# Optimization experiments

Hardware: AMD Instinct MI355X
Metric: run time of the kernel (lower is better)

Reference implementation:

```python
import jax, jax.numpy as jnp
import numpy as np

N = 50000          # nodes
E = 800000         # edges (avg degree 16)
H, D = 4, 32       # heads, per-head channels; hidden = H*D = 128
DIMS_IN = [32, 128, 128]


def setup_inputs() -> dict:
    key = jax.random.key(0)
    ks = jax.random.split(key, 40)
    inp = {}
    inp["x"] = jax.random.normal(ks[0], (N, 32), jnp.float32)
    inp["edge_index"] = jax.random.randint(ks[1], (2, E), 0, N, dtype=jnp.int32)
    i = 2
    for l, din in enumerate(DIMS_IN):
        for nm in ["q", "k", "v", "s"]:
            inp[f"W{nm}{l}"] = jax.random.normal(ks[i], (din, H * D), jnp.float32) / np.float32(np.sqrt(din)); i += 1
            inp[f"b{nm}{l}"] = jax.random.normal(ks[i], (H * D,), jnp.float32) * 0.01; i += 1
    inp["Wf"] = jax.random.normal(ks[i], (H * D, 1), jnp.float32) / np.float32(np.sqrt(H * D)); i += 1
    inp["bf"] = jax.random.normal(ks[i], (1,), jnp.float32) * 0.01
    return inp


def _transformer_conv(x, src, dst, Wq, bq, Wk, bk, Wv, bv, Ws, bs):
    """PyG TransformerConv (concat=True, root_weight=True, beta=False, eval mode)."""
    n = x.shape[0]
    q = (x @ Wq + bq).reshape(n, H, D)   # queries at nodes
    k = (x @ Wk + bk).reshape(n, H, D)
    v = (x @ Wv + bv).reshape(n, H, D)
    # per-edge attention score: q at destination, k at source
    s = jnp.einsum("ehd,ehd->eh", q[dst], k[src]) / np.float32(np.sqrt(D))  # [E,H]
    # segment softmax over incoming edges of each destination node
    m = jax.ops.segment_max(s, dst, num_segments=n)          # [N,H]
    e = jnp.exp(s - m[dst])                                  # [E,H]
    den = jax.ops.segment_sum(e, dst, num_segments=n)        # [N,H]
    alpha = e / den[dst]                                     # [E,H]
    agg = jax.ops.segment_sum(alpha[:, :, None] * v[src], dst, num_segments=n)  # [N,H,D]
    return agg.reshape(n, H * D) + (x @ Ws + bs)             # skip connection


def reference(x, edge_index,
              Wq0, bq0, Wk0, bk0, Wv0, bv0, Ws0, bs0,
              Wq1, bq1, Wk1, bk1, Wv1, bv1, Ws1, bs1,
              Wq2, bq2, Wk2, bk2, Wv2, bv2, Ws2, bs2,
              Wf, bf):
    src, dst = edge_index[0], edge_index[1]
    layers = [
        (Wq0, bq0, Wk0, bk0, Wv0, bv0, Ws0, bs0),
        (Wq1, bq1, Wk1, bk1, Wv1, bv1, Ws1, bs1),
        (Wq2, bq2, Wk2, bk2, Wv2, bv2, Ws2, bs2),
    ]
    h = x
    for p in layers:
        h = jax.nn.relu(_transformer_conv(h, src, dst, *p))
    out = jax.nn.sigmoid(h @ Wf + bf)  # [N,1]
    return out
```

## Files before the change

kernel.cpp:

```cpp
#include <hip/hip_runtime.h>
#include <hip/hip_bf16.h>
#include <cstdint>
#include <cstddef>

typedef __attribute__((ext_vector_type(8))) short bf16x8;
typedef __attribute__((ext_vector_type(4))) float f32x4;
typedef __attribute__((ext_vector_type(2))) float f32x2;

#define MAXD 64

__device__ __forceinline__ unsigned short f2bs(float f){
  __hip_bfloat16 h = __float2bfloat16(f);
  return *(unsigned short*)&h;
}
__device__ __forceinline__ unsigned short f2bs_trunc(float f){
  return (unsigned short)(__float_as_uint(f) >> 16);
}
__device__ __forceinline__ float bflo(unsigned int u){ return __uint_as_float(u << 16); }
__device__ __forceinline__ float bfhi(unsigned int u){ return __uint_as_float(u & 0xffff0000u); }
__device__ __forceinline__ f32x2 b2f2(unsigned int u){
  return (f32x2){ __uint_as_float(u << 16), __uint_as_float(u & 0xffff0000u) };
}

struct PrepArgs {
  const float* w[8];
  unsigned short* o[8];
  int* cnt;
  int n;
};

__global__ void prep_kernel(PrepArgs a){
  int m = blockIdx.y;
  if (m < 8){
    int e = blockIdx.x*256 + threadIdx.x;
    int n  = e >> 6;
    int k2 = e & 63;
    const float* W = a.w[m];
    unsigned int lo = __float_as_uint(W[(2*k2)  *128 + n]) >> 16;
    unsigned int hi = __float_as_uint(W[(2*k2+1)*128 + n]) & 0xffff0000u;
    ((unsigned int*)a.o[m])[e] = lo | hi;
  } else {
    for (int i = blockIdx.x*256 + threadIdx.x; i < a.n; i += 32*256) a.cnt[i] = 0;
  }
}

__global__ __launch_bounds__(256)
void scatter_gemm0(const int* __restrict__ src, const int* __restrict__ dst, int E,
                   int* __restrict__ cnt, int* __restrict__ adj, int SB, int gb,
                   const float* __restrict__ x, int nn,
                   const float* __restrict__ W0, const float* __restrict__ W1,
                   const float* __restrict__ W2, const float* __restrict__ W3,
                   const float* __restrict__ b0, const float* __restrict__ b1,
                   const float* __restrict__ b2, const float* __restrict__ b3,
                   unsigned short* __restrict__ Q, unsigned short* __restrict__ KV,
                   unsigned short* __restrict__ S)
{
  __shared__ __align__(16) unsigned short wt[128*40];
  int t = threadIdx.x;
  if ((int)blockIdx.x < SB){
    int e = blockIdx.x*256 + t;
    if (e < E){
      int d = dst[e];
      int slot = atomicAdd(&cnt[d], 1);
      if (slot < MAXD) adj[d*MAXD + slot] = src[e];
    }
    return;
  }
  int b2i  = blockIdx.x - SB;
  int msel = b2i / gb;
  int tile = b2i % gb;
  const float* W = (msel==0)?W0:(msel==1)?W1:(msel==2)?W2:W3;
  const float* B = (msel==0)?b0:(msel==1)?b1:(msel==2)?b2:b3;

  for (int idx = t; idx < 4096; idx += 256){
    int k = idx >> 7, n = idx & 127;
    wt[n*40 + k] = f2bs_trunc(W[k*128 + n]);
  }

  int lane = t & 63, wv = t >> 6;
  int m0 = tile*64 + wv*16;
  int n16 = lane & 15, quad = lane >> 4;

  int arow = min(m0 + n16, nn-1);
  const float* xr = x + (size_t)arow*32 + quad*8;
  float4 a0 = *(const float4*)xr;
  float4 a1 = *(const float4*)(xr + 4);
  bf16x8 af;
  af[0]=(short)f2bs_trunc(a0.x); af[1]=(short)f2bs_trunc(a0.y);
  af[2]=(short)f2bs_trunc(a0.z); af[3]=(short)f2bs_trunc(a0.w);
  af[4]=(short)f2bs_trunc(a1.x); af[5]=(short)f2bs_trunc(a1.y);
  af[6]=(short)f2bs_trunc(a1.z); af[7]=(short)f2bs_trunc(a1.w);

  __syncthreads();

  f32x4 acc[8];
  #pragma unroll
  for (int c=0;c<8;c++) acc[c] = (f32x4){0.f,0.f,0.f,0.f};
  #pragma unroll
  for (int c = 0; c < 8; c++){
    bf16x8 bf = *(const bf16x8*)&wt[(c*16 + n16)*40 + quad*8];
    acc[c] = __builtin_amdgcn_mfma_f32_16x16x32_bf16(af, bf, acc[c], 0, 0, 0);
  }

  unsigned short* O = (msel==0) ? Q : (msel==3) ? S : KV;
  int ostride = (msel==1 || msel==2) ? 256 : 128;
  int ooff    = (msel==2) ? 128 : 0;
  #pragma unroll
  for (int c = 0; c < 8; c++){
    int col = c*16 + n16;
    float bias = B[col];
    #pragma unroll
    for (int r = 0; r < 4; r++){
      int row = m0 + quad*4 + r;
      if (row < nn) O[(size_t)row*ostride + ooff + col] = f2bs(acc[c][r] + bias);
    }
  }
}

__global__ __launch_bounds__(256)
void gemm4_mfma(const unsigned short* __restrict__ X, int nn,
                const unsigned short* __restrict__ T0, const unsigned short* __restrict__ T1,
                const unsigned short* __restrict__ T2, const unsigned short* __restrict__ T3,
                const float* __restrict__ b0, const float* __restrict__ b1,
                const float* __restrict__ b2, const float* __restrict__ b3,
                unsigned short* __restrict__ Q, unsigned short* __restrict__ KV,
                unsigned short* __restrict__ S)
{
  constexpr int DIN = 128, KP = DIN + 8;
  __shared__ __align__(16) unsigned short wt[128*KP];
  int t = threadIdx.x;
  int msel = blockIdx.y;
  const unsigned short* WT = (msel==0)?T0:(msel==1)?T1:(msel==2)?T2:T3;
  const float* B = (msel==0)?b0:(msel==1)?b1:(msel==2)?b2:b3;

  {
    const int NU = 128*DIN/8;
    for (int u = t; u < NU; u += 256){
      uint4 v = ((const uint4*)WT)[u];
      int n = u / (DIN/8), b = u % (DIN/8);
      *(uint4*)&wt[n*KP + b*8] = v;
    }
  }

  int lane = t & 63, wv = t >> 6;
  int m0 = blockIdx.x*64 + wv*16;
  int n16 = lane & 15, quad = lane >> 4;

  bf16x8 af[DIN/32];
  {
    const unsigned short* xrow = X + (size_t)(m0 + n16)*DIN + quad*8;
    #pragma unroll
    for (int s = 0; s < DIN/32; s++) af[s] = *(const bf16x8*)(xrow + s*32);
  }

  __syncthreads();

  f32x4 acc[8];
  #pragma unroll
  for (int c=0;c<8;c++) acc[c] = (f32x4){0.f,0.f,0.f,0.f};
  #pragma unroll
  for (int s = 0; s < DIN/32; s++){
    #pragma unroll
    for (int c = 0; c < 8; c++){
      bf16x8 bf = *(const bf16x8*)&wt[(c*16 + n16)*KP + s*32 + quad*8];
      acc[c] = __builtin_amdgcn_mfma_f32_16x16x32_bf16(af[s], bf, acc[c], 0, 0, 0);
    }
  }

  unsigned short* O = (msel==0) ? Q : (msel==3) ? S : KV;
  int ostride = (msel==1 || msel==2) ? 256 : 128;
  int ooff    = (msel==2) ? 128 : 0;
  #pragma unroll
  for (int c = 0; c < 8; c++){
    int col = c*16 + n16;
    float bias = B[col];
    #pragma unroll
    for (int r = 0; r < 4; r++){
      int row = m0 + quad*4 + r;
      if (row < nn) O[(size_t)row*ostride + ooff + col] = f2bs(acc[c][r] + bias);
    }
  }
}

template<bool FINAL>
__global__ __launch_bounds__(256)
void attn_kernel(const unsigned short* __restrict__ q,  const unsigned short* __restrict__ kv,
                 const unsigned short* __restrict__ skip,
                 const int* __restrict__ cnt, const int* __restrict__ adj,
                 unsigned short* __restrict__ hout,
                 const float* __restrict__ Wf, const float* __restrict__ bfp,
                 float* __restrict__ out, int nn)
{
  int lane = threadIdx.x & 63, wid = threadIdx.x >> 6;
  int n = blockIdx.x*4 + wid;
  if (n >= nn) return;
  int p = lane & 15, g = lane >> 4;
  const float RS = 0.17677669529663687f;

  f32x2 qv[4];
  { uint4 qu = *(const uint4*)(q + (size_t)n*128 + p*8);
    qv[0]=b2f2(qu.x); qv[1]=b2f2(qu.y); qv[2]=b2f2(qu.z); qv[3]=b2f2(qu.w); }

  int dg = min(cnt[n], MAXD);
  float m = -INFINITY, l = 0.f;
  f32x2 acc[4] = {{0.f,0.f},{0.f,0.f},{0.f,0.f},{0.f,0.f}};

  if (dg > 0){
    int cn = dg;
    int idx = adj[n*MAXD + min(lane, cn-1)];
    int nit = (cn + 7) >> 3;

    bool a0 = 2*g < cn, a1 = 2*g + 1 < cn;
    int s0 = __shfl(idx, min(2*g    , cn-1), 64);
    int s1 = __shfl(idx, min(2*g + 1, cn-1), 64);
    uint4 ku0 = *(const uint4*)(kv + (size_t)s0*256 + p*8);
    uint4 ku1 = *(const uint4*)(kv + (size_t)s1*256 + p*8);
    uint4 vu0 = *(const uint4*)(kv + (size_t)s0*256 + 128 + p*8);
    uint4 vu1 = *(const uint4*)(kv + (size_t)s1*256 + 128 + p*8);

    for (int it = 0; it < nit; ++it){
      int jn0 = (it+1)*8 + 2*g;
      bool b0 = jn0 < cn, b1 = jn0 + 1 < cn;
      int t0 = __shfl(idx, min(jn0    , cn-1), 64);
      int t1 = __shfl(idx, min(jn0 + 1, cn-1), 64);
      uint4 kn0={0,0,0,0}, kn1={0,0,0,0}, vn0={0,0,0,0}, vn1={0,0,0,0};
      if (it + 1 < nit){
        kn0 = *(const uint4*)(kv + (size_t)t0*256 + p*8);
        kn1 = *(const uint4*)(kv + (size_t)t1*256 + p*8);
        vn0 = *(const uint4*)(kv + (size_t)t0*256 + 128 + p*8);
        vn1 = *(const uint4*)(kv + (size_t)t1*256 + 128 + p*8);
      }
      f32x2 d0v = qv[0]*b2f2(ku0.x);
      d0v = __builtin_elementwise_fma(qv[1], b2f2(ku0.y), d0v);
      d0v = __builtin_elementwise_fma(qv[2], b2f2(ku0.z), d0v);
      d0v = __builtin_elementwise_fma(qv[3], b2f2(ku0.w), d0v);
      f32x2 d1v = qv[0]*b2f2(ku1.x);
      d1v = __builtin_elementwise_fma(qv[1], b2f2(ku1.y), d1v);
      d1v = __builtin_elementwise_fma(qv[2], b2f2(ku1.z), d1v);
      d1v = __builtin_elementwise_fma(qv[3], b2f2(ku1.w), d1v);
      float d0 = d0v.x + d0v.y;
      float d1 = d1v.x + d1v.y;
      d0 += __shfl_xor(d0, 1, 64); d0 += __shfl_xor(d0, 2, 64);
      d1 += __shfl_xor(d1, 1, 64); d1 += __shfl_xor(d1, 2, 64);
      float f0 = a0 ? d0*RS : -INFINITY;
      float f1 = a1 ? d1*RS : -INFINITY;

      float nm = fmaxf(m, fmaxf(f0, f1));
      float r  = __expf(fmaxf(m  - nm, -80.f));
      float w0 = __expf(fmaxf(f0 - nm, -80.f));
      float w1 = __expf(fmaxf(f1 - nm, -80.f));
      m = nm;
      l = l*r + (w0 + w1);
      f32x2 rr  = {r , r };
      f32x2 w0v = {w0, w0};
      f32x2 w1v = {w1, w1};
      acc[0] = __builtin_elementwise_fma(w1v, b2f2(vu1.x),
               __builtin_elementwise_fma(w0v, b2f2(vu0.x), acc[0]*rr));
      acc[1] = __builtin_elementwise_fma(w1v, b2f2(vu1.y),
               __builtin_elementwise_fma(w0v, b2f2(vu0.y), acc[1]*rr));
      acc[2] = __builtin_elementwise_fma(w1v, b2f2(vu1.z),
               __builtin_elementwise_fma(w0v, b2f2(vu0.z), acc[2]*rr));
      acc[3] = __builtin_elementwise_fma(w1v, b2f2(vu1.w),
               __builtin_elementwise_fma(w0v, b2f2(vu0.w), acc[3]*rr));
      ku0=kn0; ku1=kn1; vu0=vn0; vu1=vn1; a0=b0; a1=b1;
    }
  }

  float m1 = fmaxf(m, __shfl_xor(m, 16, 64));
  float M  = fmaxf(m1, __shfl_xor(m1, 32, 64));
  float sc = __expf(fmaxf(m - M, -80.f));
  float lp = l * sc;
  lp += __shfl_xor(lp, 16, 64);
  float L = lp + __shfl_xor(lp, 32, 64);
  f32x2 scv = {sc, sc};
  float o[8];
  #pragma unroll
  for (int i=0;i<4;i++){
    f32x2 a = acc[i]*scv;
    a.x += __shfl_xor(a.x, 16, 64); a.y += __shfl_xor(a.y, 16, 64);
    a.x += __shfl_xor(a.x, 32, 64); a.y += __shfl_xor(a.y, 32, 64);
    o[2*i] = a.x; o[2*i+1] = a.y;
  }
  float inv = (L > 0.f) ? 1.f/L : 0.f;
  float sk[8];
  { uint4 su = *(const uint4*)(skip + (size_t)n*128 + p*8);
    sk[0]=bflo(su.x); sk[1]=bfhi(su.x); sk[2]=bflo(su.y); sk[3]=bfhi(su.y);
    sk[4]=bflo(su.z); sk[5]=bfhi(su.z); sk[6]=bflo(su.w); sk[7]=bfhi(su.w); }
  #pragma unroll
  for (int i=0;i<8;i++) o[i] = fmaxf(fmaf(o[i], inv, sk[i]), 0.f);

  if constexpr (!FINAL){
    if (g == 0){
      uint4 st;
      st.x = (unsigned)f2bs(o[0]) | ((unsigned)f2bs(o[1])<<16);
      st.y = (unsigned)f2bs(o[2]) | ((unsigned)f2bs(o[3])<<16);
      st.z = (unsigned)f2bs(o[4]) | ((unsigned)f2bs(o[5])<<16);
      st.w = (unsigned)f2bs(o[6]) | ((unsigned)f2bs(o[7])<<16);
      *(uint4*)(hout + (size_t)n*128 + p*8) = st;
    }
  } else {
    float4 w0 = *(const float4*)(Wf + p*8);
    float4 w1 = *(const float4*)(Wf + p*8 + 4);
    float pd = o[0]*w0.x;
    pd = fmaf(o[1], w0.y, pd); pd = fmaf(o[2], w0.z, pd); pd = fmaf(o[3], w0.w, pd);
    pd = fmaf(o[4], w1.x, pd); pd = fmaf(o[5], w1.y, pd);
    pd = fmaf(o[6], w1.z, pd); pd = fmaf(o[7], w1.w, pd);
    pd += __shfl_xor(pd, 1, 64);
    pd += __shfl_xor(pd, 2, 64);
    pd += __shfl_xor(pd, 4, 64);
    pd += __shfl_xor(pd, 8, 64);
    if (lane == 0){
      float z = pd + bfp[0];
      out[n] = 1.f / (1.f + __expf(-z));
    }
  }
}

extern "C" void kernel_launch(void* const* d_in, const int* in_sizes, int n_in,
                              void* d_out, int out_size, void* d_ws, size_t ws_size,
                              hipStream_t stream) {
  const int N = in_sizes[0] / 32;
  const int E = in_sizes[1] / 2;
  const float* x = (const float*)d_in[0];
  const int* ei  = (const int*)d_in[1];
  const int* src = ei;
  const int* dst = ei + E;
  auto Wp = [&](int i){ return (const float*)d_in[i]; };
  const int NP = N + 64;

  char* p = (char*)d_ws;
  auto alloc = [&](size_t b){ char* r = p; p += (b + 255) & ~(size_t)255; return (void*)r; };
  unsigned short* F0  = (unsigned short*)alloc((size_t)NP*128*2);
  unsigned short* F1  = (unsigned short*)alloc((size_t)NP*128*2);
  unsigned short* Qb  = (unsigned short*)alloc((size_t)NP*128*2);
  unsigned short* KVb = (unsigned short*)alloc((size_t)NP*256*2);
  unsigned short* WT[8];
  for (int i = 0; i < 8; i++) WT[i] = (unsigned short*)alloc((size_t)128*128*2);
  int* cnt = (int*)alloc((size_t)N*4);
  int* adj = (int*)alloc((size_t)N*MAXD*4);

  PrepArgs pa;
  const int widx[8] = {10,12,14,16, 18,20,22,24};
  for (int i = 0; i < 8; i++){ pa.w[i] = Wp(widx[i]); pa.o[i] = WT[i]; }
  pa.cnt = cnt; pa.n = N;
  prep_kernel<<<dim3(32,9), 256, 0, stream>>>(pa);

  int SB = (E + 255) / 256;
  int gb = (N + 63) / 64;
  int ab = (N + 3) / 4;

  scatter_gemm0<<<SB + 4*gb, 256, 0, stream>>>(src, dst, E, cnt, adj, SB, gb,
      x, N, Wp(2),Wp(4),Wp(6),Wp(8), Wp(3),Wp(5),Wp(7),Wp(9), Qb, KVb, F0);
  attn_kernel<false><<<ab, 256, 0, stream>>>(Qb, KVb, F0, cnt, adj, F0,
      nullptr, nullptr, nullptr, N);
  gemm4_mfma<<<dim3(gb,4), 256, 0, stream>>>(F0, N,
      WT[0],WT[1],WT[2],WT[3], Wp(11),Wp(13),Wp(15),Wp(17), Qb, KVb, F1);
  attn_kernel<false><<<ab, 256, 0, stream>>>(Qb, KVb, F1, cnt, adj, F1,
      nullptr, nullptr, nullptr, N);
  gemm4_mfma<<<dim3(gb,4), 256, 0, stream>>>(F1, N,
      WT[4],WT[5],WT[6],WT[7], Wp(19),Wp(21),Wp(23),Wp(25), Qb, KVb, F0);
  attn_kernel<true><<<ab, 256, 0, stream>>>(Qb, KVb, F0, cnt, adj, nullptr,
      Wp(26), Wp(27), (float*)d_out, N);
}
```

Before: 416.3 us.

## Fuse all layers into one persistent cooperative kernel with grid syncs

Replaces the seven separate launches (weight prep, scatter plus first GEMM, three attention passes, two GEMMs) with a single cooperative kernel. Blocks grid-stride through each phase and are separated by grid.sync barriers. The aim is to remove per-launch overhead and the tail idle between kernels. In exchange, the grid is capped by occupancy, at most 4 blocks per CU with a 34 KB LDS buffer held throughout. That may reduce latency hiding in the gather-heavy attention phases, and each grid-wide barrier adds its own cost.

```diff
diff --git a/kernel.cpp b/kernel.cpp
--- a/kernel.cpp
+++ b/kernel.cpp
@@ -1,7 +1,10 @@
 #include <hip/hip_runtime.h>
+#include <hip/hip_cooperative_groups.h>
 #include <hip/hip_bf16.h>
 #include <cstdint>
 #include <cstddef>
+
+namespace cg = cooperative_groups;
 
 typedef __attribute__((ext_vector_type(8))) short bf16x8;
 typedef __attribute__((ext_vector_type(4))) float f32x4;
@@ -22,61 +25,29 @@
   return (f32x2){ __uint_as_float(u << 16), __uint_as_float(u & 0xffff0000u) };
 }
 
-struct PrepArgs {
-  const float* w[8];
-  unsigned short* o[8];
-  int* cnt;
-  int n;
+struct MegaArgs {
+  const int* src; const int* dst; int E;
+  const float* x; int N;
+  const float* W0[4]; const float* B0[4];
+  const float* W12[8];
+  const float* B1[4]; const float* B2[4];
+  unsigned short* WT[8];
+  const float* Wf; const float* bfp;
+  unsigned short *F0, *F1, *Q, *KV;
+  int* cnt; int* adj;
+  float* out;
 };
 
-__global__ void prep_kernel(PrepArgs a){
-  int m = blockIdx.y;
-  if (m < 8){
-    int e = blockIdx.x*256 + threadIdx.x;
-    int n  = e >> 6;
-    int k2 = e & 63;
-    const float* W = a.w[m];
-    unsigned int lo = __float_as_uint(W[(2*k2)  *128 + n]) >> 16;
-    unsigned int hi = __float_as_uint(W[(2*k2+1)*128 + n]) & 0xffff0000u;
-    ((unsigned int*)a.o[m])[e] = lo | hi;
-  } else {
-    for (int i = blockIdx.x*256 + threadIdx.x; i < a.n; i += 32*256) a.cnt[i] = 0;
-  }
-}
-
-__global__ __launch_bounds__(256)
-void scatter_gemm0(const int* __restrict__ src, const int* __restrict__ dst, int E,
-                   int* __restrict__ cnt, int* __restrict__ adj, int SB, int gb,
-                   const float* __restrict__ x, int nn,
-                   const float* __restrict__ W0, const float* __restrict__ W1,
-                   const float* __restrict__ W2, const float* __restrict__ W3,
-                   const float* __restrict__ b0, const float* __restrict__ b1,
-                   const float* __restrict__ b2, const float* __restrict__ b3,
-                   unsigned short* __restrict__ Q, unsigned short* __restrict__ KV,
-                   unsigned short* __restrict__ S)
+__device__ __forceinline__ void gemm0_tile(unsigned short* wt, const float* __restrict__ x, int nn,
+    const float* __restrict__ W, const float* __restrict__ B,
+    unsigned short* __restrict__ O, int ostride, int ooff, int tile)
 {
-  __shared__ __align__(16) unsigned short wt[128*40];
   int t = threadIdx.x;
-  if ((int)blockIdx.x < SB){
-    int e = blockIdx.x*256 + t;
-    if (e < E){
-      int d = dst[e];
-      int slot = atomicAdd(&cnt[d], 1);
-      if (slot < MAXD) adj[d*MAXD + slot] = src[e];
-    }
-    return;
-  }
-  int b2i  = blockIdx.x - SB;
-  int msel = b2i / gb;
-  int tile = b2i % gb;
-  const float* W = (msel==0)?W0:(msel==1)?W1:(msel==2)?W2:W3;
-  const float* B = (msel==0)?b0:(msel==1)?b1:(msel==2)?b2:b3;
-
+  __syncthreads();
   for (int idx = t; idx < 4096; idx += 256){
     int k = idx >> 7, n = idx & 127;
     wt[n*40 + k] = f2bs_trunc(W[k*128 + n]);
   }
-
   int lane = t & 63, wv = t >> 6;
   int m0 = tile*64 + wv*16;
   int n16 = lane & 15, quad = lane >> 4;
@@ -101,10 +72,6 @@
     bf16x8 bf = *(const bf16x8*)&wt[(c*16 + n16)*40 + quad*8];
     acc[c] = __builtin_amdgcn_mfma_f32_16x16x32_bf16(af, bf, acc[c], 0, 0, 0);
   }
-
-  unsigned short* O = (msel==0) ? Q : (msel==3) ? S : KV;
-  int ostride = (msel==1 || msel==2) ? 256 : 128;
-  int ooff    = (msel==2) ? 128 : 0;
   #pragma unroll
   for (int c = 0; c < 8; c++){
     int col = c*16 + n16;
@@ -117,59 +84,42 @@
   }
 }
 
-__global__ __launch_bounds__(256)
-void gemm4_mfma(const unsigned short* __restrict__ X, int nn,
-                const unsigned short* __restrict__ T0, const unsigned short* __restrict__ T1,
-                const unsigned short* __restrict__ T2, const unsigned short* __restrict__ T3,
-                const float* __restrict__ b0, const float* __restrict__ b1,
-                const float* __restrict__ b2, const float* __restrict__ b3,
-                unsigned short* __restrict__ Q, unsigned short* __restrict__ KV,
-                unsigned short* __restrict__ S)
+__device__ __forceinline__ void gemm128_tile(unsigned short* wt, const unsigned short* __restrict__ X,
+    int nn, const unsigned short* __restrict__ WT, const float* __restrict__ B,
+    unsigned short* __restrict__ O, int ostride, int ooff, int tile)
 {
-  constexpr int DIN = 128, KP = DIN + 8;
-  __shared__ __align__(16) unsigned short wt[128*KP];
   int t = threadIdx.x;
-  int msel = blockIdx.y;
-  const unsigned short* WT = (msel==0)?T0:(msel==1)?T1:(msel==2)?T2:T3;
-  const float* B = (msel==0)?b0:(msel==1)?b1:(msel==2)?b2:b3;
-
+  __syncthreads();
   {
-    const int NU = 128*DIN/8;
-    for (int u = t; u < NU; u += 256){
+    for (int u = t; u < 2048; u += 256){
       uint4 v = ((const uint4*)WT)[u];
-      int n = u / (DIN/8), b = u % (DIN/8);
-      *(uint4*)&wt[n*KP + b*8] = v;
-    }
-  }
-
+      int n = u >> 4, b = u & 15;
+      *(uint4*)&wt[n*136 + b*8] = v;
+    }
+  }
   int lane = t & 63, wv = t >> 6;
-  int m0 = blockIdx.x*64 + wv*16;
+  int m0 = tile*64 + wv*16;
   int n16 = lane & 15, quad = lane >> 4;
 
-  bf16x8 af[DIN/32];
+  bf16x8 af[4];
   {
-    const unsigned short* xrow = X + (size_t)(m0 + n16)*DIN + quad*8;
+    const unsigned short* xrow = X + (size_t)(m0 + n16)*128 + quad*8;
     #pragma unroll
-    for (int s = 0; s < DIN/32; s++) af[s] = *(const bf16x8*)(xrow + s*32);
-  }
-
+    for (int s = 0; s < 4; s++) af[s] = *(const bf16x8*)(xrow + s*32);
+  }
   __syncthreads();
 
   f32x4 acc[8];
   #pragma unroll
   for (int c=0;c<8;c++) acc[c] = (f32x4){0.f,0.f,0.f,0.f};
   #pragma unroll
-  for (int s = 0; s < DIN/32; s++){
+  for (int s = 0; s < 4; s++){
     #pragma unroll
     for (int c = 0; c < 8; c++){
-      bf16x8 bf = *(const bf16x8*)&wt[(c*16 + n16)*KP + s*32 + quad*8];
+      bf16x8 bf = *(const bf16x8*)&wt[(c*16 + n16)*136 + s*32 + quad*8];
       acc[c] = __builtin_amdgcn_mfma_f32_16x16x32_bf16(af[s], bf, acc[c], 0, 0, 0);
     }
   }
-
-  unsigned short* O = (msel==0) ? Q : (msel==3) ? S : KV;
-  int ostride = (msel==1 || msel==2) ? 256 : 128;
-  int ooff    = (msel==2) ? 128 : 0;
   #pragma unroll
   for (int c = 0; c < 8; c++){
     int col = c*16 + n16;
@@ -182,17 +132,13 @@
   }
 }
 
-template<bool FINAL>
-__global__ __launch_bounds__(256)
-void attn_kernel(const unsigned short* __restrict__ q,  const unsigned short* __restrict__ kv,
-                 const unsigned short* __restrict__ skip,
-                 const int* __restrict__ cnt, const int* __restrict__ adj,
-                 unsigned short* __restrict__ hout,
-                 const float* __restrict__ Wf, const float* __restrict__ bfp,
-                 float* __restrict__ out, int nn)
+__device__ __forceinline__ void attn_node(int n, int nn,
+    const unsigned short* __restrict__ q, const unsigned short* __restrict__ kv,
+    const unsigned short* __restrict__ skip, const int* __restrict__ cnt,
+    const int* __restrict__ adj, unsigned short* __restrict__ hout,
+    const float* __restrict__ Wf, const float* __restrict__ bfp,
+    float* __restrict__ out, bool final_, int lane)
 {
-  int lane = threadIdx.x & 63, wid = threadIdx.x >> 6;
-  int n = blockIdx.x*4 + wid;
   if (n >= nn) return;
   int p = lane & 15, g = lane >> 4;
   const float RS = 0.17677669529663687f;
@@ -276,10 +222,10 @@
   float o[8];
   #pragma unroll
   for (int i=0;i<4;i++){
-    f32x2 a = acc[i]*scv;
-    a.x += __shfl_xor(a.x, 16, 64); a.y += __shfl_xor(a.y, 16, 64);
-    a.x += __shfl_xor(a.x, 32, 64); a.y += __shfl_xor(a.y, 32, 64);
-    o[2*i] = a.x; o[2*i+1] = a.y;
+    f32x2 aa = acc[i]*scv;
+    aa.x += __shfl_xor(aa.x, 16, 64); aa.y += __shfl_xor(aa.y, 16, 64);
+    aa.x += __shfl_xor(aa.x, 32, 64); aa.y += __shfl_xor(aa.y, 32, 64);
+    o[2*i] = aa.x; o[2*i+1] = aa.y;
   }
   float inv = (L > 0.f) ? 1.f/L : 0.f;
   float sk[8];
@@ -289,7 +235,7 @@
   #pragma unroll
   for (int i=0;i<8;i++) o[i] = fmaxf(fmaf(o[i], inv, sk[i]), 0.f);
 
-  if constexpr (!FINAL){
+  if (!final_){
     if (g == 0){
       uint4 st;
       st.x = (unsigned)f2bs(o[0]) | ((unsigned)f2bs(o[1])<<16);
@@ -316,6 +262,81 @@
   }
 }
 
+__global__ __launch_bounds__(256, 4)
+void mega_kernel(MegaArgs a)
+{
+  __shared__ __align__(16) unsigned short wt[128*136];
+  cg::grid_group grid = cg::this_grid();
+  const int G = gridDim.x;
+  int t = threadIdx.x;
+  int lane = t & 63, wid = t >> 6;
+
+  for (int u = blockIdx.x*256 + t; u < 8*8192; u += G*256){
+    int m = u >> 13, e = u & 8191;
+    int n = e >> 6, k2 = e & 63;
+    const float* W = a.W12[m];
+    unsigned int lo = __float_as_uint(W[(2*k2)  *128 + n]) >> 16;
+    unsigned int hi = __float_as_uint(W[(2*k2+1)*128 + n]) & 0xffff0000u;
+    ((unsigned int*)a.WT[m])[e] = lo | hi;
+  }
+  for (int i = blockIdx.x*256 + t; i < a.N; i += G*256) a.cnt[i] = 0;
+  grid.sync();
+
+  int SB = (a.E + 255) >> 8;
+  int gb = (a.N + 63) >> 6;
+  for (int b = blockIdx.x; b < SB + 4*gb; b += G){
+    if (b < SB){
+      int e = b*256 + t;
+      if (e < a.E){
+        int d = a.dst[e];
+        int slot = atomicAdd(&a.cnt[d], 1);
+        if (slot < MAXD) a.adj[d*MAXD + slot] = a.src[e];
+      }
+    } else {
+      int b2 = b - SB;
+      int msel = b2 / gb, tile = b2 % gb;
+      unsigned short* O = (msel==0) ? a.Q : (msel==3) ? a.F0 : a.KV;
+      int ostride = (msel==1 || msel==2) ? 256 : 128;
+      int ooff    = (msel==2) ? 128 : 0;
+      gemm0_tile(wt, a.x, a.N, a.W0[msel], a.B0[msel], O, ostride, ooff, tile);
+    }
+  }
+  grid.sync();
+
+  int ab = (a.N + 3) >> 2;
+  for (int i = blockIdx.x; i < ab; i += G)
+    attn_node(i*4 + wid, a.N, a.Q, a.KV, a.F0, a.cnt, a.adj, a.F0,
+              nullptr, nullptr, nullptr, false, lane);
+  grid.sync();
+
+  for (int b = blockIdx.x; b < 4*gb; b += G){
+    int msel = b / gb, tile = b % gb;
+    unsigned short* O = (msel==0) ? a.Q : (msel==3) ? a.F1 : a.KV;
+    int ostride = (msel==1 || msel==2) ? 256 : 128;
+    int ooff    = (msel==2) ? 128 : 0;
+    gemm128_tile(wt, a.F0, a.N, a.WT[msel], a.B1[msel], O, ostride, ooff, tile);
+  }
+  grid.sync();
+
+  for (int i = blockIdx.x; i < ab; i += G)
+    attn_node(i*4 + wid, a.N, a.Q, a.KV, a.F1, a.cnt, a.adj, a.F1,
+              nullptr, nullptr, nullptr, false, lane);
+  grid.sync();
+
+  for (int b = blockIdx.x; b < 4*gb; b += G){
+    int msel = b / gb, tile = b % gb;
+    unsigned short* O = (msel==0) ? a.Q : (msel==3) ? a.F0 : a.KV;
+    int ostride = (msel==1 || msel==2) ? 256 : 128;
+    int ooff    = (msel==2) ? 128 : 0;
+    gemm128_tile(wt, a.F1, a.N, a.WT[4+msel], a.B2[msel], O, ostride, ooff, tile);
+  }
+  grid.sync();
+
+  for (int i = blockIdx.x; i < ab; i += G)
+    attn_node(i*4 + wid, a.N, a.Q, a.KV, a.F0, a.cnt, a.adj, nullptr,
+              a.Wf, a.bfp, a.out, true, lane);
+}
+
 extern "C" void kernel_launch(void* const* d_in, const int* in_sizes, int n_in,
                               void* d_out, int out_size, void* d_ws, size_t ws_size,
                               hipStream_t stream) {
@@ -323,8 +344,6 @@
   const int E = in_sizes[1] / 2;
   const float* x = (const float*)d_in[0];
   const int* ei  = (const int*)d_in[1];
-  const int* src = ei;
-  const int* dst = ei + E;
   auto Wp = [&](int i){ return (const float*)d_in[i]; };
   const int NP = N + 64;
 
@@ -339,26 +358,28 @@
   int* cnt = (int*)alloc((size_t)N*4);
   int* adj = (int*)alloc((size_t)N*MAXD*4);
 
-  PrepArgs pa;
-  const int widx[8] = {10,12,14,16, 18,20,22,24};
-  for (int i = 0; i < 8; i++){ pa.w[i] = Wp(widx[i]); pa.o[i] = WT[i]; }
-  pa.cnt = cnt; pa.n = N;
-  prep_kernel<<<dim3(32,9), 256, 0, stream>>>(pa);
-
-  int SB = (E + 255) / 256;
-  int gb = (N + 63) / 64;
-  int ab = (N + 3) / 4;
-
-  scatter_gemm0<<<SB + 4*gb, 256, 0, stream>>>(src, dst, E, cnt, adj, SB, gb,
-      x, N, Wp(2),Wp(4),Wp(6),Wp(8), Wp(3),Wp(5),Wp(7),Wp(9), Qb, KVb, F0);
-  attn_kernel<false><<<ab, 256, 0, stream>>>(Qb, KVb, F0, cnt, adj, F0,
-      nullptr, nullptr, nullptr, N);
-  gemm4_mfma<<<dim3(gb,4), 256, 0, stream>>>(F0, N,
-      WT[0],WT[1],WT[2],WT[3], Wp(11),Wp(13),Wp(15),Wp(17), Qb, KVb, F1);
-  attn_kernel<false><<<ab, 256, 0, stream>>>(Qb, KVb, F1, cnt, adj, F1,
-      nullptr, nullptr, nullptr, N);
-  gemm4_mfma<<<dim3(gb,4), 256, 0, stream>>>(F1, N,
-      WT[4],WT[5],WT[6],WT[7], Wp(19),Wp(21),Wp(23),Wp(25), Qb, KVb, F0);
-  attn_kernel<true><<<ab, 256, 0, stream>>>(Qb, KVb, F0, cnt, adj, nullptr,
-      Wp(26), Wp(27), (float*)d_out, N);
-}
+  MegaArgs ma;
+  ma.src = ei; ma.dst = ei + E; ma.E = E;
+  ma.x = x; ma.N = N;
+  const int w0i[4] = {2,4,6,8};
+  const int w1i[4] = {10,12,14,16};
+  const int w2i[4] = {18,20,22,24};
+  for (int i = 0; i < 4; i++){
+    ma.W0[i]  = Wp(w0i[i]); ma.B0[i] = Wp(w0i[i]+1);
+    ma.W12[i]   = Wp(w1i[i]); ma.B1[i] = Wp(w1i[i]+1);
+    ma.W12[4+i] = Wp(w2i[i]); ma.B2[i] = Wp(w2i[i]+1);
+  }
+  for (int i = 0; i < 8; i++) ma.WT[i] = WT[i];
+  ma.Wf = Wp(26); ma.bfp = Wp(27);
+  ma.F0 = F0; ma.F1 = F1; ma.Q = Qb; ma.KV = KVb;
+  ma.cnt = cnt; ma.adj = adj;
+  ma.out = (float*)d_out;
+
+  int maxB = 0;
+  hipOccupancyMaxActiveBlocksPerMultiprocessor(&maxB, mega_kernel, 256, 0);
+  int G = (maxB > 0) ? maxB * 256 : 768;
+  if (G > 2048) G = 2048;
+
+  void* params[] = { &ma };
+  hipLaunchCooperativeKernel((void*)mega_kernel, dim3(G), dim3(256), params, 0, stream);
+}
```

Result: slower. 898.6 us (+115.9%).

## Partition adjacency scatter by destination range and fold weight prep into fused kernel

Applied to the files above, without the earlier changes.

The edge scatter now has each block handle a 2048-edge chunk restricted to one of 8 destination-node ranges. Blocks working on the same range run close together, so atomics and adjacency writes are meant to stay in a narrower, more cache-friendly address window. The weight transpose/bf16 conversion for layers 1-2 moves into the same fused launch as the scatter and the layer-0 GEMM, and the counter zeroing becomes its own small kernel. The cost is that every edge's dst is read 8 times, which adds load traffic.

```diff
diff --git a/kernel.cpp b/kernel.cpp
--- a/kernel.cpp
+++ b/kernel.cpp
@@ -22,97 +22,110 @@
   return (f32x2){ __uint_as_float(u << 16), __uint_as_float(u & 0xffff0000u) };
 }
 
-struct PrepArgs {
-  const float* w[8];
-  unsigned short* o[8];
-  int* cnt;
-  int n;
+__global__ void zero_cnt_kernel(int* __restrict__ p, int n){
+  int i = blockIdx.x*256 + threadIdx.x;
+  if (i < n) p[i] = 0;
+}
+
+struct FatArgs {
+  const int* src; const int* dst; int E;
+  int* cnt; int* adj;
+  int SBP, GB;
+  const float* x; int N;
+  const float* W0[4]; const float* B0[4];
+  const float* W12[8];
+  unsigned short* WT[8];
+  unsigned short *Q, *KV, *S;
 };
 
-__global__ void prep_kernel(PrepArgs a){
-  int m = blockIdx.y;
-  if (m < 8){
-    int e = blockIdx.x*256 + threadIdx.x;
-    int n  = e >> 6;
-    int k2 = e & 63;
-    const float* W = a.w[m];
-    unsigned int lo = __float_as_uint(W[(2*k2)  *128 + n]) >> 16;
-    unsigned int hi = __float_as_uint(W[(2*k2+1)*128 + n]) & 0xffff0000u;
-    ((unsigned int*)a.o[m])[e] = lo | hi;
-  } else {
-    for (int i = blockIdx.x*256 + threadIdx.x; i < a.n; i += 32*256) a.cnt[i] = 0;
-  }
-}
-
 __global__ __launch_bounds__(256)
-void scatter_gemm0(const int* __restrict__ src, const int* __restrict__ dst, int E,
-                   int* __restrict__ cnt, int* __restrict__ adj, int SB, int gb,
-                   const float* __restrict__ x, int nn,
-                   const float* __restrict__ W0, const float* __restrict__ W1,
-                   const float* __restrict__ W2, const float* __restrict__ W3,
-                   const float* __restrict__ b0, const float* __restrict__ b1,
-                   const float* __restrict__ b2, const float* __restrict__ b3,
-                   unsigned short* __restrict__ Q, unsigned short* __restrict__ KV,
-                   unsigned short* __restrict__ S)
+void fat_kernel(FatArgs a)
 {
   __shared__ __align__(16) unsigned short wt[128*40];
   int t = threadIdx.x;
-  if ((int)blockIdx.x < SB){
-    int e = blockIdx.x*256 + t;
-    if (e < E){
-      int d = dst[e];
-      int slot = atomicAdd(&cnt[d], 1);
-      if (slot < MAXD) adj[d*MAXD + slot] = src[e];
+  int b = blockIdx.x;
+
+  if (b < a.SBP){
+    int p = b & 7, c = b >> 3;
+    int base = c*2048;
+    int plo = ( p      * a.N) / 8;
+    int phi = ((p + 1) * a.N) / 8;
+    #pragma unroll
+    for (int i = 0; i < 8; i++){
+      int e = base + t + i*256;
+      if (e < a.E){
+        int d = a.dst[e];
+        if (d >= plo && d < phi){
+          int slot = atomicAdd(&a.cnt[d], 1);
+          if (slot < MAXD) a.adj[d*MAXD + slot] = a.src[e];
+        }
+      }
     }
     return;
   }
-  int b2i  = blockIdx.x - SB;
-  int msel = b2i / gb;
-  int tile = b2i % gb;
-  const float* W = (msel==0)?W0:(msel==1)?W1:(msel==2)?W2:W3;
-  const float* B = (msel==0)?b0:(msel==1)?b1:(msel==2)?b2:b3;
-
-  for (int idx = t; idx < 4096; idx += 256){
-    int k = idx >> 7, n = idx & 127;
-    wt[n*40 + k] = f2bs_trunc(W[k*128 + n]);
-  }
-
-  int lane = t & 63, wv = t >> 6;
-  int m0 = tile*64 + wv*16;
-  int n16 = lane & 15, quad = lane >> 4;
-
-  int arow = min(m0 + n16, nn-1);
-  const float* xr = x + (size_t)arow*32 + quad*8;
-  float4 a0 = *(const float4*)xr;
-  float4 a1 = *(const float4*)(xr + 4);
-  bf16x8 af;
-  af[0]=(short)f2bs_trunc(a0.x); af[1]=(short)f2bs_trunc(a0.y);
-  af[2]=(short)f2bs_trunc(a0.z); af[3]=(short)f2bs_trunc(a0.w);
-  af[4]=(short)f2bs_trunc(a1.x); af[5]=(short)f2bs_trunc(a1.y);
-  af[6]=(short)f2bs_trunc(a1.z); af[7]=(short)f2bs_trunc(a1.w);
-
-  __syncthreads();
-
-  f32x4 acc[8];
-  #pragma unroll
-  for (int c=0;c<8;c++) acc[c] = (f32x4){0.f,0.f,0.f,0.f};
-  #pragma unroll
-  for (int c = 0; c < 8; c++){
-    bf16x8 bf = *(const bf16x8*)&wt[(c*16 + n16)*40 + quad*8];
-    acc[c] = __builtin_amdgcn_mfma_f32_16x16x32_bf16(af, bf, acc[c], 0, 0, 0);
-  }
-
-  unsigned short* O = (msel==0) ? Q : (msel==3) ? S : KV;
-  int ostride = (msel==1 || msel==2) ? 256 : 128;
-  int ooff    = (msel==2) ? 128 : 0;
-  #pragma unroll
-  for (int c = 0; c < 8; c++){
-    int col = c*16 + n16;
-    float bias = B[col];
-    #pragma unroll
-    for (int r = 0; r < 4; r++){
-      int row = m0 + quad*4 + r;
-      if (row < nn) O[(size_t)row*ostride + ooff + col] = f2bs(acc[c][r] + bias);
+  b -= a.SBP;
+
+  if (b < 4*a.GB){
+    int msel = b / a.GB, tile = b % a.GB;
+    const float* W = a.W0[msel];
+    const float* B = a.B0[msel];
+    for (int idx = t; idx < 4096; idx += 256){
+      int k = idx >> 7, n = idx & 127;
+      wt[n*40 + k] = f2bs_trunc(W[k*128 + n]);
+    }
+    int lane = t & 63, wv = t >> 6;
+    int m0 = tile*64 + wv*16;
+    int n16 = lane & 15, quad = lane >> 4;
+
+    int arow = min(m0 + n16, a.N-1);
+    const float* xr = a.x + (size_t)arow*32 + quad*8;
+    float4 a0 = *(const float4*)xr;
+    float4 a1 = *(const float4*)(xr + 4);
+    bf16x8 af;
+    af[0]=(short)f2bs_trunc(a0.x); af[1]=(short)f2bs_trunc(a0.y);
+    af[2]=(short)f2bs_trunc(a0.z); af[3]=(short)f2bs_trunc(a0.w);
+    af[4]=(short)f2bs_trunc(a1.x); af[5]=(short)f2bs_trunc(a1.y);
+    af[6]=(short)f2bs_trunc(a1.z); af[7]=(short)f2bs_trunc(a1.w);
+
+    __syncthreads();
+
+    f32x4 acc[8];
+    #pragma unroll
+    for (int c2=0;c2<8;c2++) acc[c2] = (f32x4){0.f,0.f,0.f,0.f};
+    #pragma unroll
+    for (int c2 = 0; c2 < 8; c2++){
+      bf16x8 bf = *(const bf16x8*)&wt[(c2*16 + n16)*40 + quad*8];
+      acc[c2] = __builtin_amdgcn_mfma_f32_16x16x32_bf16(af, bf, acc[c2], 0, 0, 0);
+    }
+
+    unsigned short* O = (msel==0) ? a.Q : (msel==3) ? a.S : a.KV;
+    int ostride = (msel==1 || msel==2) ? 256 : 128;
+    int ooff    = (msel==2) ? 128 : 0;
+    #pragma unroll
+    for (int c2 = 0; c2 < 8; c2++){
+      int col = c2*16 + n16;
+      float bias = B[col];
+      #pragma unroll
+      for (int r = 0; r < 4; r++){
+        int row = m0 + quad*4 + r;
+        if (row < a.N) O[(size_t)row*ostride + ooff + col] = f2bs(acc[c2][r] + bias);
+      }
+    }
+    return;
+  }
+  b -= 4*a.GB;
+
+  {
+    int m = b >> 2, part = b & 3;
+    const float* W = a.W12[m];
+    unsigned int* O = (unsigned int*)a.WT[m];
+    #pragma unroll
+    for (int i = 0; i < 8; i++){
+      int e = part*2048 + t + i*256;
+      int n = e >> 6, k2 = e & 63;
+      unsigned int lo = __float_as_uint(W[(2*k2)  *128 + n]) >> 16;
+      unsigned int hi = __float_as_uint(W[(2*k2+1)*128 + n]) & 0xffff0000u;
+      O[e] = lo | hi;
     }
   }
 }
@@ -276,10 +289,10 @@
   float o[8];
   #pragma unroll
   for (int i=0;i<4;i++){
-    f32x2 a = acc[i]*scv;
-    a.x += __shfl_xor(a.x, 16, 64); a.y += __shfl_xor(a.y, 16, 64);
-    a.x += __shfl_xor(a.x, 32, 64); a.y += __shfl_xor(a.y, 32, 64);
-    o[2*i] = a.x; o[2*i+1] = a.y;
+    f32x2 aa = acc[i]*scv;
+    aa.x += __shfl_xor(aa.x, 16, 64); aa.y += __shfl_xor(aa.y, 16, 64);
+    aa.x += __shfl_xor(aa.x, 32, 64); aa.y += __shfl_xor(aa.y, 32, 64);
+    o[2*i] = aa.x; o[2*i+1] = aa.y;
   }
   float inv = (L > 0.f) ? 1.f/L : 0.f;
   float sk[8];
@@ -323,8 +336,6 @@
   const int E = in_sizes[1] / 2;
   const float* x = (const float*)d_in[0];
   const int* ei  = (const int*)d_in[1];
-  const int* src = ei;
-  const int* dst = ei + E;
   auto Wp = [&](int i){ return (const float*)d_in[i]; };
   const int NP = N + 64;
 
@@ -339,18 +350,29 @@
   int* cnt = (int*)alloc((size_t)N*4);
   int* adj = (int*)alloc((size_t)N*MAXD*4);
 
-  PrepArgs pa;
-  const int widx[8] = {10,12,14,16, 18,20,22,24};
-  for (int i = 0; i < 8; i++){ pa.w[i] = Wp(widx[i]); pa.o[i] = WT[i]; }
-  pa.cnt = cnt; pa.n = N;
-  prep_kernel<<<dim3(32,9), 256, 0, stream>>>(pa);
-
-  int SB = (E + 255) / 256;
-  int gb = (N + 63) / 64;
+  zero_cnt_kernel<<<(N+255)/256, 256, 0, stream>>>(cnt, N);
+
+  FatArgs fa;
+  fa.src = ei; fa.dst = ei + E; fa.E = E;
+  fa.cnt = cnt; fa.adj = adj;
+  int chunks = (E + 2047) / 2048;
+  fa.SBP = chunks * 8;
+  fa.GB  = (N + 63) / 64;
+  fa.x = x; fa.N = N;
+  const int w0i[4] = {2,4,6,8};
+  const int w1i[4] = {10,12,14,16};
+  const int w2i[4] = {18,20,22,24};
+  for (int i = 0; i < 4; i++){
+    fa.W0[i] = Wp(w0i[i]); fa.B0[i] = Wp(w0i[i]+1);
+    fa.W12[i]   = Wp(w1i[i]);
+    fa.W12[4+i] = Wp(w2i[i]);
+  }
+  for (int i = 0; i < 8; i++) fa.WT[i] = WT[i];
+  fa.Q = Qb; fa.KV = KVb; fa.S = F0;
+  fat_kernel<<<fa.SBP + 4*fa.GB + 32, 256, 0, stream>>>(fa);
+
+  int gb = fa.GB;
   int ab = (N + 3) / 4;
-
-  scatter_gemm0<<<SB + 4*gb, 256, 0, stream>>>(src, dst, E, cnt, adj, SB, gb,
-      x, N, Wp(2),Wp(4),Wp(6),Wp(8), Wp(3),Wp(5),Wp(7),Wp(9), Qb, KVb, F0);
   attn_kernel<false><<<ab, 256, 0, stream>>>(Qb, KVb, F0, cnt, adj, F0,
       nullptr, nullptr, nullptr, N);
   gemm4_mfma<<<dim3(gb,4), 256, 0, stream>>>(F0, N,
```

Result: faster. 404.5 us (-2.8%).
